# Kernel tuning notes

Hardware: AMD Instinct MI355X
Metric: run time of the kernel (lower is better)

Reference implementation:

```python
import jax, jax.numpy as jnp
import numpy as np

T, H, N = 4096, 2048, 1024  # seq_length, d_model, d_hidden
MAX_PHASE = 6.28


def setup_inputs() -> dict:
    key = jax.random.key(0)
    ks = jax.random.split(key, 9)
    inputs = jax.random.normal(ks[0], (T, H), dtype=jnp.float32)
    # LRU init (exp_param=True, r_min=0, r_max=1): lambda = exp(-exp(nu) + i*exp(theta))
    u1 = jax.random.uniform(ks[1], (N,), dtype=jnp.float32)
    u2 = jax.random.uniform(ks[2], (N,), dtype=jnp.float32)
    nu = jnp.log(-0.5 * jnp.log(u1))            # log-parameterized decay
    theta = jnp.log(MAX_PHASE * u2)             # log-parameterized phase
    # gamma_log = log(sqrt(1 - |lambda|^2)), |lambda| = exp(-exp(nu))
    gamma_log = 0.5 * jnp.log(1.0 - jnp.exp(-2.0 * jnp.exp(nu)) + 1e-8)
    B_re = jax.random.normal(ks[3], (N, H), dtype=jnp.float32) / np.sqrt(2 * H)
    B_im = jax.random.normal(ks[4], (N, H), dtype=jnp.float32) / np.sqrt(2 * H)
    C_re = jax.random.normal(ks[5], (H, N), dtype=jnp.float32) / np.sqrt(N)
    C_im = jax.random.normal(ks[6], (H, N), dtype=jnp.float32) / np.sqrt(N)
    D = jax.random.normal(ks[7], (H,), dtype=jnp.float32)
    return {"inputs": inputs, "nu": nu, "theta": theta, "gamma_log": gamma_log,
            "B_re": B_re, "B_im": B_im, "C_re": C_re, "C_im": C_im, "D": D}


def _binary_operator_diag(q_i, q_j):
    A_i, b_i = q_i
    A_j, b_j = q_j
    return (A_j * A_i, A_j * b_i + b_j)


def reference(inputs, nu, theta, gamma_log, B_re, B_im, C_re, C_im, D):
    # diag_lambda = exp(-exp(nu) + i*exp(theta))   (exp_param=True)
    diag_lambda = jnp.exp(-jnp.exp(nu) + 1j * jnp.exp(theta))      # [N] complex64
    gamma = jnp.exp(gamma_log)                                      # [N]
    B_norm = (B_re + 1j * B_im) * gamma[:, None]                    # [N, H] complex
    # Bu_t = B_norm @ u_t  ->  [T, N]
    Bu = inputs.astype(jnp.complex64) @ B_norm.T
    Lam = jnp.broadcast_to(diag_lambda[None, :], Bu.shape)          # [T, N]
    # parallel scan of diagonal linear recurrence h_t = lambda * h_{t-1} + Bu_t
    _, h = jax.lax.associative_scan(_binary_operator_diag, (Lam, Bu))
    C = C_re + 1j * C_im                                            # [H, N]
    # y_t = Re(C @ h_t) + D * u_t
    y = (h @ C.T).real + D[None, :] * inputs                        # [T, H]
    return y
```

## Files before the change

kernel.cpp:

```cpp
#include <hip/hip_runtime.h>
#include <math.h>

#define T_DIM 4096
#define H_DIM 2048
#define N_DIM 1024
#define N2    2048
#define KK    2048
#define CHUNK 64
#define NCHUNK (T_DIM / CHUNK)
#define NT    (KK / 64)

using u16    = unsigned short;
using u16x4  = __attribute__((ext_vector_type(4))) u16;
using bf16x8 = __attribute__((ext_vector_type(8))) short;
using f32x4  = __attribute__((ext_vector_type(4))) float;

typedef const __attribute__((address_space(1))) u16 glob_u16;
typedef __attribute__((address_space(3))) u16 lds_u16;

__device__ inline void gload16(const u16* g, u16* l) {
    __builtin_amdgcn_global_load_lds((glob_u16*)g, (lds_u16*)l, 16, 0, 0);
}

__device__ inline u16 f2bf(float x) {
    unsigned u = __builtin_bit_cast(unsigned, x);
    u += 0x7fffu + ((u >> 16) & 1u);
    return (u16)(u >> 16);
}
__device__ inline float bf2f(u16 x) {
    return __builtin_bit_cast(float, (unsigned)x << 16);
}

__global__ __launch_bounds__(256) void cvt_u_k(const float* __restrict__ X,
                                               u16* __restrict__ Y) {
    size_t i = ((size_t)blockIdx.x * 256 + threadIdx.x) * 4;
    float4 v = *(const float4*)(X + i);
    u16x4 o = { f2bf(v.x), f2bf(v.y), f2bf(v.z), f2bf(v.w) };
    *(u16x4*)(Y + i) = o;
}

__global__ __launch_bounds__(256) void cvt_b_k(const float* __restrict__ Bre,
                                               const float* __restrict__ Bim,
                                               const float* __restrict__ glog,
                                               u16* __restrict__ Bcat) {
    size_t i = ((size_t)blockIdx.x * 256 + threadIdx.x) * 4;
    int n = (int)(i >> 11);
    size_t h = i & 2047;
    int nn = n & (N_DIM - 1);
    float g = expf(glog[nn]);
    const float* src = (n < N_DIM ? Bre : Bim) + (size_t)nn * H_DIM + h;
    float4 v = *(const float4*)src;
    u16x4 o = { f2bf(v.x * g), f2bf(v.y * g), f2bf(v.z * g), f2bf(v.w * g) };
    *(u16x4*)(Bcat + i) = o;
}

__global__ __launch_bounds__(256) void cvt_c_k(const float* __restrict__ Cre,
                                               const float* __restrict__ Cim,
                                               u16* __restrict__ Ccat) {
    size_t i = ((size_t)blockIdx.x * 256 + threadIdx.x) * 4;
    int hrow = (int)(i >> 11);
    int n = (int)(i & 2047);
    float sgn = 1.f;
    const float* src;
    if (n < N_DIM) src = Cre + (size_t)hrow * N_DIM + n;
    else { src = Cim + (size_t)hrow * N_DIM + (n - N_DIM); sgn = -1.f; }
    float4 v = *(const float4*)src;
    u16x4 o = { f2bf(v.x * sgn), f2bf(v.y * sgn), f2bf(v.z * sgn), f2bf(v.w * sgn) };
    *(u16x4*)(Ccat + i) = o;
}

template <int EPI>
__global__ __launch_bounds__(512, 1) void gemm_pipe(
    const u16* __restrict__ A, const u16* __restrict__ B,
    float* __restrict__ C, const float* __restrict__ D,
    const u16* __restrict__ Ubf)
{
    __shared__ u16 lds[65536];

    const int tid  = threadIdx.x;
    const int wave = tid >> 6, lane = tid & 63;
    const int nbid = (blockIdx.x & 7) * 32 + (blockIdx.x >> 3);
    const int bm = nbid >> 4;
    const int bn = nbid & 15;
    const size_t row0 = (size_t)bm * 256;
    const size_t col0 = (size_t)bn * 128;
    const int wr = wave >> 1, wc = wave & 1;
    const int fr = lane & 15, fq = lane >> 4;

    const int srow = tid >> 3;
    const int skc  = (tid & 7) ^ (srow & 7);
    const u16* aSrc = A + (row0 + srow) * KK + skc * 8;
    const u16* bSrc = B + (col0 + srow) * KK + skc * 8;

    const int aBase = (wr * 64 + fr) * 64;
    const int bBase = (wc * 64 + fr) * 64;
    const int swz0 = ((fq)     ^ (fr & 7)) * 8;
    const int swz1 = ((4 + fq) ^ (fr & 7)) * 8;

    f32x4 acc[4][4] = {};

    auto STAGE_A = [&](int buf, int kt) {
#pragma unroll
        for (int u = 0; u < 4; ++u)
            gload16(aSrc + (size_t)u * 64 * KK + kt * 64,
                    &lds[buf * 16384 + u * 4096 + wave * 512]);
    };
    auto STAGE_B = [&](int buf, int kt) {
#pragma unroll
        for (int u = 0; u < 2; ++u)
            gload16(bSrc + (size_t)u * 64 * KK + kt * 64,
                    &lds[49152 + buf * 8192 + u * 4096 + wave * 512]);
    };

    bf16x8 fa[4], fb[4], ga[4], gb[4];

    auto READ_F = [&](const u16* Ab, const u16* Bb, int swz) {
#pragma unroll
        for (int m = 0; m < 4; ++m) fa[m] = *(const bf16x8*)&Ab[aBase + m * 1024 + swz];
#pragma unroll
        for (int n = 0; n < 4; ++n) fb[n] = *(const bf16x8*)&Bb[bBase + n * 1024 + swz];
    };
    auto READ_G = [&](const u16* Ab, const u16* Bb, int swz) {
#pragma unroll
        for (int m = 0; m < 4; ++m) ga[m] = *(const bf16x8*)&Ab[aBase + m * 1024 + swz];
#pragma unroll
        for (int n = 0; n < 4; ++n) gb[n] = *(const bf16x8*)&Bb[bBase + n * 1024 + swz];
    };
    auto MFMA_F = [&]() {
        __builtin_amdgcn_s_setprio(1);
#pragma unroll
        for (int m = 0; m < 4; ++m)
#pragma unroll
            for (int n = 0; n < 4; ++n)
                acc[m][n] = __builtin_amdgcn_mfma_f32_16x16x32_bf16(
                    fa[m], fb[n], acc[m][n], 0, 0, 0);
        __builtin_amdgcn_s_setprio(0);
    };
    auto MFMA_G = [&]() {
        __builtin_amdgcn_s_setprio(1);
#pragma unroll
        for (int m = 0; m < 4; ++m)
#pragma unroll
            for (int n = 0; n < 4; ++n)
                acc[m][n] = __builtin_amdgcn_mfma_f32_16x16x32_bf16(
                    ga[m], gb[n], acc[m][n], 0, 0, 0);
        __builtin_amdgcn_s_setprio(0);
    };

    STAGE_A(0, 0); STAGE_B(0, 0); STAGE_A(1, 1);
    asm volatile("s_waitcnt vmcnt(4)" ::: "memory");
    __builtin_amdgcn_s_barrier();
    READ_F(&lds[0], &lds[49152], swz0);

    int a_cur = 0;
    for (int t = 0; t < NT; ++t) {
        const u16* Ab = &lds[a_cur * 16384];
        const u16* Bb = &lds[49152 + (t & 1) * 8192];

        if (t + 1 < NT) STAGE_B((t + 1) & 1, t + 1);
        MFMA_F();
        if (t + 2 < NT) {
            int a_nxt = a_cur - 1; if (a_nxt < 0) a_nxt = 2;
            STAGE_A(a_nxt, t + 2);
        }
        READ_G(Ab, Bb, swz1);
        MFMA_G();

        if (t + 1 < NT) {
            if (t + 2 < NT) asm volatile("s_waitcnt vmcnt(4)" ::: "memory");
            else            asm volatile("s_waitcnt vmcnt(0)" ::: "memory");
            __builtin_amdgcn_s_barrier();
            int a_n = a_cur + 1; if (a_n == 3) a_n = 0;
            READ_F(&lds[a_n * 16384], &lds[49152 + ((t + 1) & 1) * 8192], swz0);
        }
        ++a_cur; if (a_cur == 3) a_cur = 0;
    }

    const int crow = (int)row0 + wr * 64 + fq * 4;
    const int ccol = (int)col0 + wc * 64 + fr;
    float dc[4];
    if constexpr (EPI) {
#pragma unroll
        for (int n = 0; n < 4; ++n) dc[n] = D[ccol + n * 16];
    }
#pragma unroll
    for (int m = 0; m < 4; ++m)
#pragma unroll
        for (int n = 0; n < 4; ++n) {
            int cc = ccol + n * 16;
#pragma unroll
            for (int j = 0; j < 4; ++j) {
                int r = crow + m * 16 + j;
                size_t p = (size_t)r * N2 + cc;
                float v = acc[m][n][j];
                if constexpr (EPI) v += dc[n] * bf2f(Ubf[p]);
                C[p] = v;
            }
        }
}

__global__ __launch_bounds__(256) void carry_pass_k(const float* __restrict__ Bu,
                                                    const float* __restrict__ nu,
                                                    const float* __restrict__ theta,
                                                    float* __restrict__ car) {
    int idx = blockIdx.x * 256 + threadIdx.x;
    int chan = idx & (N_DIM - 1);
    int chunk = idx >> 10;
    float a = expf(nu[chan]), b = expf(theta[chan]);
    float m = expf(-a), s, c;
    __sincosf(b, &s, &c);
    float lr = m * c, li = m * s;
    float hr = 0.f, hi = 0.f;
    size_t base = (size_t)chunk * CHUNK * N2 + chan;
    for (int i = 0; i < CHUNK; ++i) {
        size_t p = base + (size_t)i * N2;
        float br = Bu[p], bi = Bu[p + N_DIM];
        float nr = fmaf(lr, hr, fmaf(-li, hi, br));
        float ni = fmaf(lr, hi, fmaf(li, hr, bi));
        hr = nr; hi = ni;
    }
    car[(size_t)chunk * N2 + chan] = hr;
    car[(size_t)chunk * N2 + N_DIM + chan] = hi;
}

__global__ __launch_bounds__(256) void scan_carry_k(float* __restrict__ car,
                                                    const float* __restrict__ nu,
                                                    const float* __restrict__ theta) {
    __shared__ float sR[NCHUNK][65], sI[NCHUNK][65];
    int tid = threadIdx.x;
    int chan0 = blockIdx.x * 64;
    for (int i = tid; i < NCHUNK * 64; i += 256) {
        int ck = i >> 6, c = i & 63;
        sR[ck][c] = car[(size_t)ck * N2 + chan0 + c];
        sI[ck][c] = car[(size_t)ck * N2 + N_DIM + chan0 + c];
    }
    __syncthreads();
    if (tid < 64) {
        int chan = chan0 + tid;
        float a = expf(nu[chan]), b = expf(theta[chan]);
        float m = expf(-(float)CHUNK * a), s, c;
        __sincosf((float)CHUNK * b, &s, &c);
        float lr = m * c, li = m * s;
        float hr = sR[0][tid], hi = sI[0][tid];
        for (int ck = 1; ck < NCHUNK; ++ck) {
            float nr = fmaf(lr, hr, fmaf(-li, hi, sR[ck][tid]));
            float ni = fmaf(lr, hi, fmaf(li, hr, sI[ck][tid]));
            hr = nr; hi = ni;
            sR[ck][tid] = hr; sI[ck][tid] = hi;
        }
    }
    __syncthreads();
    for (int i = tid; i < NCHUNK * 64; i += 256) {
        int ck = i >> 6, c = i & 63;
        car[(size_t)ck * N2 + chan0 + c] = sR[ck][c];
        car[(size_t)ck * N2 + N_DIM + chan0 + c] = sI[ck][c];
    }
}

__global__ __launch_bounds__(256) void scan_out_k(const float* __restrict__ Bu,
                                                  const float* __restrict__ car,
                                                  const float* __restrict__ nu,
                                                  const float* __restrict__ theta,
                                                  u16* __restrict__ Hbf) {
    int idx = blockIdx.x * 256 + threadIdx.x;
    int chan = idx & (N_DIM - 1);
    int chunk = idx >> 10;
    float a = expf(nu[chan]), b = expf(theta[chan]);
    float m = expf(-a), s, c;
    __sincosf(b, &s, &c);
    float lr = m * c, li = m * s;
    float hr = 0.f, hi = 0.f;
    if (chunk > 0) {
        size_t cp = (size_t)(chunk - 1) * N2 + chan;
        hr = car[cp]; hi = car[cp + N_DIM];
    }
    size_t base = (size_t)chunk * CHUNK * N2 + chan;
    for (int i = 0; i < CHUNK; ++i) {
        size_t p = base + (size_t)i * N2;
        float br = Bu[p], bi = Bu[p + N_DIM];
        float nr = fmaf(lr, hr, fmaf(-li, hi, br));
        float ni = fmaf(lr, hi, fmaf(li, hr, bi));
        hr = nr; hi = ni;
        Hbf[p] = f2bf(hr);
        Hbf[p + N_DIM] = f2bf(hi);
    }
}

extern "C" void kernel_launch(void* const* d_in, const int* in_sizes, int n_in,
                              void* d_out, int out_size, void* d_ws, size_t ws_size,
                              hipStream_t stream) {
    const float* U     = (const float*)d_in[0];
    const float* nu    = (const float*)d_in[1];
    const float* theta = (const float*)d_in[2];
    const float* glog  = (const float*)d_in[3];
    const float* Bre   = (const float*)d_in[4];
    const float* Bim   = (const float*)d_in[5];
    const float* Cre   = (const float*)d_in[6];
    const float* Cim   = (const float*)d_in[7];
    const float* Dp    = (const float*)d_in[8];
    float* Y = (float*)d_out;

    u16* Ubf  = (u16*)d_ws;
    u16* Bcat = Ubf + (size_t)T_DIM * H_DIM;
    u16* Ccat = Bcat + (size_t)N2 * H_DIM;
    u16* Hbf  = Ccat + (size_t)H_DIM * N2;
    float* Bu = (float*)(Hbf + (size_t)T_DIM * N2);
    float* car = Bu + (size_t)T_DIM * N2;

    cvt_u_k<<<(T_DIM * H_DIM / 4) / 256, 256, 0, stream>>>(U, Ubf);
    cvt_b_k<<<((size_t)N2 * H_DIM / 4) / 256, 256, 0, stream>>>(Bre, Bim, glog, Bcat);
    cvt_c_k<<<((size_t)H_DIM * N2 / 4) / 256, 256, 0, stream>>>(Cre, Cim, Ccat);

    gemm_pipe<0><<<256, 512, 0, stream>>>(Ubf, Bcat, Bu, nullptr, nullptr);

    carry_pass_k<<<(NCHUNK * N_DIM) / 256, 256, 0, stream>>>(Bu, nu, theta, car);
    scan_carry_k<<<N_DIM / 64, 256, 0, stream>>>(car, nu, theta);
    scan_out_k<<<(NCHUNK * N_DIM) / 256, 256, 0, stream>>>(Bu, car, nu, theta, Hbf);

    gemm_pipe<1><<<256, 512, 0, stream>>>(Hbf, Ccat, Y, Dp, Ubf);
}
```

Baseline: 114.9 us.

## Split K across wave pairs in GEMM with LDS reduction of partial accumulators

The GEMM kernel now assigns the two k-halves of each 64-wide K tile to separate waves. Each wave computes a 128x64 output sub-tile over half the K slice, and the two partial accumulators are reduced through LDS before the epilogue. The F/G double-buffered register prefetch is removed, and launch bounds now request two blocks per SM. The intent is fewer LDS fragment reads per MFMA, since each wave reuses its B fragments across 8 A rows, plus more latency hiding. The costs are higher register pressure (128 accumulator floats per lane), the loss of the register-level prefetch overlap, and an extra LDS reduction with a barrier. The 128KB LDS allocation likely still prevents two blocks from sharing an SM.

```diff
diff --git a/kernel.cpp b/kernel.cpp
--- a/kernel.cpp
+++ b/kernel.cpp
@@ -70,7 +70,7 @@
 }
 
 template <int EPI>
-__global__ __launch_bounds__(512, 1) void gemm_pipe(
+__global__ __launch_bounds__(512, 2) void gemm_pipe(
     const u16* __restrict__ A, const u16* __restrict__ B,
     float* __restrict__ C, const float* __restrict__ D,
     const u16* __restrict__ Ubf)
@@ -84,7 +84,9 @@
     const int bn = nbid & 15;
     const size_t row0 = (size_t)bm * 256;
     const size_t col0 = (size_t)bn * 128;
-    const int wr = wave >> 1, wc = wave & 1;
+    const int kg = wave & 1;
+    const int wc = (wave >> 1) & 1;
+    const int wr = wave >> 2;
     const int fr = lane & 15, fq = lane >> 4;
 
     const int srow = tid >> 3;
@@ -92,12 +94,11 @@
     const u16* aSrc = A + (row0 + srow) * KK + skc * 8;
     const u16* bSrc = B + (col0 + srow) * KK + skc * 8;
 
-    const int aBase = (wr * 64 + fr) * 64;
-    const int bBase = (wc * 64 + fr) * 64;
-    const int swz0 = ((fq)     ^ (fr & 7)) * 8;
-    const int swz1 = ((4 + fq) ^ (fr & 7)) * 8;
-
-    f32x4 acc[4][4] = {};
+    const int slot = ((kg * 4 + fq) ^ (fr & 7)) * 8;
+    const int aOff = (wr * 128 + fr) * 64 + slot;
+    const int bOff = (wc * 64 + fr) * 64 + slot;
+
+    f32x4 acc[8][4] = {};
 
     auto STAGE_A = [&](int buf, int kt) {
 #pragma unroll
@@ -112,91 +113,82 @@
                     &lds[49152 + buf * 8192 + u * 4096 + wave * 512]);
     };
 
-    bf16x8 fa[4], fb[4], ga[4], gb[4];
-
-    auto READ_F = [&](const u16* Ab, const u16* Bb, int swz) {
-#pragma unroll
-        for (int m = 0; m < 4; ++m) fa[m] = *(const bf16x8*)&Ab[aBase + m * 1024 + swz];
-#pragma unroll
-        for (int n = 0; n < 4; ++n) fb[n] = *(const bf16x8*)&Bb[bBase + n * 1024 + swz];
-    };
-    auto READ_G = [&](const u16* Ab, const u16* Bb, int swz) {
-#pragma unroll
-        for (int m = 0; m < 4; ++m) ga[m] = *(const bf16x8*)&Ab[aBase + m * 1024 + swz];
-#pragma unroll
-        for (int n = 0; n < 4; ++n) gb[n] = *(const bf16x8*)&Bb[bBase + n * 1024 + swz];
-    };
-    auto MFMA_F = [&]() {
+    STAGE_A(0, 0); STAGE_B(0, 0); STAGE_A(1, 1);
+    asm volatile("s_waitcnt vmcnt(4)" ::: "memory");
+    __builtin_amdgcn_s_barrier();
+
+    int a_cur = 0;
+    for (int t = 0; t < NT; ++t) {
+        const u16* Ab = &lds[a_cur * 16384];
+        const u16* Bb = &lds[49152 + (t & 1) * 8192];
+
+        bf16x8 fb[4], fa[8];
+#pragma unroll
+        for (int n = 0; n < 4; ++n) fb[n] = *(const bf16x8*)&Bb[bOff + n * 1024];
+#pragma unroll
+        for (int m = 0; m < 8; ++m) fa[m] = *(const bf16x8*)&Ab[aOff + m * 1024];
+
+        if (t + 1 < NT) STAGE_B((t + 1) & 1, t + 1);
+        if (t + 2 < NT) {
+            int a_nxt = a_cur + 2; if (a_nxt >= 3) a_nxt -= 3;
+            STAGE_A(a_nxt, t + 2);
+        }
+
         __builtin_amdgcn_s_setprio(1);
 #pragma unroll
-        for (int m = 0; m < 4; ++m)
+        for (int m = 0; m < 8; ++m)
 #pragma unroll
             for (int n = 0; n < 4; ++n)
                 acc[m][n] = __builtin_amdgcn_mfma_f32_16x16x32_bf16(
                     fa[m], fb[n], acc[m][n], 0, 0, 0);
         __builtin_amdgcn_s_setprio(0);
-    };
-    auto MFMA_G = [&]() {
-        __builtin_amdgcn_s_setprio(1);
-#pragma unroll
-        for (int m = 0; m < 4; ++m)
-#pragma unroll
-            for (int n = 0; n < 4; ++n)
-                acc[m][n] = __builtin_amdgcn_mfma_f32_16x16x32_bf16(
-                    ga[m], gb[n], acc[m][n], 0, 0, 0);
-        __builtin_amdgcn_s_setprio(0);
-    };
-
-    STAGE_A(0, 0); STAGE_B(0, 0); STAGE_A(1, 1);
-    asm volatile("s_waitcnt vmcnt(4)" ::: "memory");
-    __builtin_amdgcn_s_barrier();
-    READ_F(&lds[0], &lds[49152], swz0);
-
-    int a_cur = 0;
-    for (int t = 0; t < NT; ++t) {
-        const u16* Ab = &lds[a_cur * 16384];
-        const u16* Bb = &lds[49152 + (t & 1) * 8192];
-
-        if (t + 1 < NT) STAGE_B((t + 1) & 1, t + 1);
-        MFMA_F();
-        if (t + 2 < NT) {
-            int a_nxt = a_cur - 1; if (a_nxt < 0) a_nxt = 2;
-            STAGE_A(a_nxt, t + 2);
-        }
-        READ_G(Ab, Bb, swz1);
-        MFMA_G();
 
         if (t + 1 < NT) {
             if (t + 2 < NT) asm volatile("s_waitcnt vmcnt(4)" ::: "memory");
             else            asm volatile("s_waitcnt vmcnt(0)" ::: "memory");
             __builtin_amdgcn_s_barrier();
-            int a_n = a_cur + 1; if (a_n == 3) a_n = 0;
-            READ_F(&lds[a_n * 16384], &lds[49152 + ((t + 1) & 1) * 8192], swz0);
         }
         ++a_cur; if (a_cur == 3) a_cur = 0;
     }
 
-    const int crow = (int)row0 + wr * 64 + fq * 4;
-    const int ccol = (int)col0 + wc * 64 + fr;
-    float dc[4];
-    if constexpr (EPI) {
-#pragma unroll
-        for (int n = 0; n < 4; ++n) dc[n] = D[ccol + n * 16];
-    }
-#pragma unroll
-    for (int m = 0; m < 4; ++m)
-#pragma unroll
-        for (int n = 0; n < 4; ++n) {
-            int cc = ccol + n * 16;
-#pragma unroll
-            for (int j = 0; j < 4; ++j) {
-                int r = crow + m * 16 + j;
-                size_t p = (size_t)r * N2 + cc;
-                float v = acc[m][n][j];
-                if constexpr (EPI) v += dc[n] * bf2f(Ubf[p]);
-                C[p] = v;
+    __builtin_amdgcn_s_barrier();
+    const int pair = wr * 2 + wc;
+    float* lf = (float*)lds;
+    if (kg == 1) {
+#pragma unroll
+        for (int i = 0; i < 32; ++i)
+            *(f32x4*)&lf[pair * 8192 + (i * 64 + lane) * 4] = acc[i >> 2][i & 3];
+    }
+    asm volatile("s_waitcnt lgkmcnt(0)" ::: "memory");
+    __builtin_amdgcn_s_barrier();
+    if (kg == 0) {
+#pragma unroll
+        for (int i = 0; i < 32; ++i) {
+            f32x4 o = *(const f32x4*)&lf[pair * 8192 + (i * 64 + lane) * 4];
+            acc[i >> 2][i & 3] += o;
+        }
+        const int crow = (int)row0 + wr * 128 + fq * 4;
+        const int ccol = (int)col0 + wc * 64 + fr;
+        float dc[4];
+        if constexpr (EPI) {
+#pragma unroll
+            for (int n = 0; n < 4; ++n) dc[n] = D[ccol + n * 16];
+        }
+#pragma unroll
+        for (int m = 0; m < 8; ++m)
+#pragma unroll
+            for (int n = 0; n < 4; ++n) {
+                int cc = ccol + n * 16;
+#pragma unroll
+                for (int j = 0; j < 4; ++j) {
+                    int r = crow + m * 16 + j;
+                    size_t p = (size_t)r * N2 + cc;
+                    float v = acc[m][n][j];
+                    if constexpr (EPI) v += dc[n] * bf2f(Ubf[p]);
+                    C[p] = v;
+                }
             }
-        }
+    }
 }
 
 __global__ __launch_bounds__(256) void carry_pass_k(const float* __restrict__ Bu,
```

Result: slower. 122.2 us (+6.3%).

## Shrink GEMM tiles to 128x128 with two blocks per CU and store Bu as bf16

Applied to the files above, without the earlier changes.

The GEMM block tile drops from 256x128 with 512 threads to 128x128 with 256 threads. LDS use falls so two blocks can share a CU, and the grid doubles to 512 blocks with the XCD remap adjusted to match. The first GEMM now writes Bu as bf16 instead of fp32, which halves the traffic for that write and for the two scan kernels that read it. The cost is less reuse per tile and extra rounding error on Bu before the recurrence.

```diff
diff --git a/kernel.cpp b/kernel.cpp
--- a/kernel.cpp
+++ b/kernel.cpp
@@ -70,19 +70,19 @@
 }
 
 template <int EPI>
-__global__ __launch_bounds__(512, 1) void gemm_pipe(
+__global__ __launch_bounds__(256, 2) void gemm_pipe(
     const u16* __restrict__ A, const u16* __restrict__ B,
-    float* __restrict__ C, const float* __restrict__ D,
+    void* __restrict__ Cout, const float* __restrict__ D,
     const u16* __restrict__ Ubf)
 {
-    __shared__ u16 lds[65536];
+    __shared__ u16 lds[40960];
 
     const int tid  = threadIdx.x;
     const int wave = tid >> 6, lane = tid & 63;
-    const int nbid = (blockIdx.x & 7) * 32 + (blockIdx.x >> 3);
+    const int nbid = (blockIdx.x & 7) * 64 + (blockIdx.x >> 3);
     const int bm = nbid >> 4;
     const int bn = nbid & 15;
-    const size_t row0 = (size_t)bm * 256;
+    const size_t row0 = (size_t)bm * 128;
     const size_t col0 = (size_t)bn * 128;
     const int wr = wave >> 1, wc = wave & 1;
     const int fr = lane & 15, fq = lane >> 4;
@@ -92,8 +92,8 @@
     const u16* aSrc = A + (row0 + srow) * KK + skc * 8;
     const u16* bSrc = B + (col0 + srow) * KK + skc * 8;
 
-    const int aBase = (wr * 64 + fr) * 64;
-    const int bBase = (wc * 64 + fr) * 64;
+    const int aOff = (wr * 64 + fr) * 64;
+    const int bOff = (wc * 64 + fr) * 64;
     const int swz0 = ((fq)     ^ (fr & 7)) * 8;
     const int swz1 = ((4 + fq) ^ (fr & 7)) * 8;
 
@@ -102,29 +102,29 @@
     auto STAGE_A = [&](int buf, int kt) {
 #pragma unroll
         for (int u = 0; u < 4; ++u)
-            gload16(aSrc + (size_t)u * 64 * KK + kt * 64,
-                    &lds[buf * 16384 + u * 4096 + wave * 512]);
+            gload16(aSrc + (size_t)u * 32 * KK + kt * 64,
+                    &lds[buf * 8192 + u * 2048 + wave * 512]);
     };
     auto STAGE_B = [&](int buf, int kt) {
 #pragma unroll
-        for (int u = 0; u < 2; ++u)
-            gload16(bSrc + (size_t)u * 64 * KK + kt * 64,
-                    &lds[49152 + buf * 8192 + u * 4096 + wave * 512]);
+        for (int u = 0; u < 4; ++u)
+            gload16(bSrc + (size_t)u * 32 * KK + kt * 64,
+                    &lds[24576 + buf * 8192 + u * 2048 + wave * 512]);
     };
 
     bf16x8 fa[4], fb[4], ga[4], gb[4];
 
     auto READ_F = [&](const u16* Ab, const u16* Bb, int swz) {
 #pragma unroll
-        for (int m = 0; m < 4; ++m) fa[m] = *(const bf16x8*)&Ab[aBase + m * 1024 + swz];
-#pragma unroll
-        for (int n = 0; n < 4; ++n) fb[n] = *(const bf16x8*)&Bb[bBase + n * 1024 + swz];
+        for (int m = 0; m < 4; ++m) fa[m] = *(const bf16x8*)&Ab[aOff + m * 1024 + swz];
+#pragma unroll
+        for (int n = 0; n < 4; ++n) fb[n] = *(const bf16x8*)&Bb[bOff + n * 1024 + swz];
     };
     auto READ_G = [&](const u16* Ab, const u16* Bb, int swz) {
 #pragma unroll
-        for (int m = 0; m < 4; ++m) ga[m] = *(const bf16x8*)&Ab[aBase + m * 1024 + swz];
-#pragma unroll
-        for (int n = 0; n < 4; ++n) gb[n] = *(const bf16x8*)&Bb[bBase + n * 1024 + swz];
+        for (int m = 0; m < 4; ++m) ga[m] = *(const bf16x8*)&Ab[aOff + m * 1024 + swz];
+#pragma unroll
+        for (int n = 0; n < 4; ++n) gb[n] = *(const bf16x8*)&Bb[bOff + n * 1024 + swz];
     };
     auto MFMA_F = [&]() {
         __builtin_amdgcn_s_setprio(1);
@@ -150,17 +150,17 @@
     STAGE_A(0, 0); STAGE_B(0, 0); STAGE_A(1, 1);
     asm volatile("s_waitcnt vmcnt(4)" ::: "memory");
     __builtin_amdgcn_s_barrier();
-    READ_F(&lds[0], &lds[49152], swz0);
+    READ_F(&lds[0], &lds[24576], swz0);
 
     int a_cur = 0;
     for (int t = 0; t < NT; ++t) {
-        const u16* Ab = &lds[a_cur * 16384];
-        const u16* Bb = &lds[49152 + (t & 1) * 8192];
+        const u16* Ab = &lds[a_cur * 8192];
+        const u16* Bb = &lds[24576 + (t & 1) * 8192];
 
         if (t + 1 < NT) STAGE_B((t + 1) & 1, t + 1);
         MFMA_F();
         if (t + 2 < NT) {
-            int a_nxt = a_cur - 1; if (a_nxt < 0) a_nxt = 2;
+            int a_nxt = a_cur + 2; if (a_nxt >= 3) a_nxt -= 3;
             STAGE_A(a_nxt, t + 2);
         }
         READ_G(Ab, Bb, swz1);
@@ -171,7 +171,7 @@
             else            asm volatile("s_waitcnt vmcnt(0)" ::: "memory");
             __builtin_amdgcn_s_barrier();
             int a_n = a_cur + 1; if (a_n == 3) a_n = 0;
-            READ_F(&lds[a_n * 16384], &lds[49152 + ((t + 1) & 1) * 8192], swz0);
+            READ_F(&lds[a_n * 8192], &lds[24576 + ((t + 1) & 1) * 8192], swz0);
         }
         ++a_cur; if (a_cur == 3) a_cur = 0;
     }
@@ -193,13 +193,15 @@
                 int r = crow + m * 16 + j;
                 size_t p = (size_t)r * N2 + cc;
                 float v = acc[m][n][j];
-                if constexpr (EPI) v += dc[n] * bf2f(Ubf[p]);
-                C[p] = v;
+                if constexpr (EPI)
+                    ((float*)Cout)[p] = v + dc[n] * bf2f(Ubf[p]);
+                else
+                    ((u16*)Cout)[p] = f2bf(v);
             }
         }
 }
 
-__global__ __launch_bounds__(256) void carry_pass_k(const float* __restrict__ Bu,
+__global__ __launch_bounds__(256) void carry_pass_k(const u16* __restrict__ Bu,
                                                     const float* __restrict__ nu,
                                                     const float* __restrict__ theta,
                                                     float* __restrict__ car) {
@@ -214,7 +216,7 @@
     size_t base = (size_t)chunk * CHUNK * N2 + chan;
     for (int i = 0; i < CHUNK; ++i) {
         size_t p = base + (size_t)i * N2;
-        float br = Bu[p], bi = Bu[p + N_DIM];
+        float br = bf2f(Bu[p]), bi = bf2f(Bu[p + N_DIM]);
         float nr = fmaf(lr, hr, fmaf(-li, hi, br));
         float ni = fmaf(lr, hi, fmaf(li, hr, bi));
         hr = nr; hi = ni;
@@ -257,7 +259,7 @@
     }
 }
 
-__global__ __launch_bounds__(256) void scan_out_k(const float* __restrict__ Bu,
+__global__ __launch_bounds__(256) void scan_out_k(const u16* __restrict__ Bu,
                                                   const float* __restrict__ car,
                                                   const float* __restrict__ nu,
                                                   const float* __restrict__ theta,
@@ -277,7 +279,7 @@
     size_t base = (size_t)chunk * CHUNK * N2 + chan;
     for (int i = 0; i < CHUNK; ++i) {
         size_t p = base + (size_t)i * N2;
-        float br = Bu[p], bi = Bu[p + N_DIM];
+        float br = bf2f(Bu[p]), bi = bf2f(Bu[p + N_DIM]);
         float nr = fmaf(lr, hr, fmaf(-li, hi, br));
         float ni = fmaf(lr, hi, fmaf(li, hr, bi));
         hr = nr; hi = ni;
@@ -304,18 +306,18 @@
     u16* Bcat = Ubf + (size_t)T_DIM * H_DIM;
     u16* Ccat = Bcat + (size_t)N2 * H_DIM;
     u16* Hbf  = Ccat + (size_t)H_DIM * N2;
-    float* Bu = (float*)(Hbf + (size_t)T_DIM * N2);
-    float* car = Bu + (size_t)T_DIM * N2;
+    u16* Bu   = Hbf + (size_t)T_DIM * N2;
+    float* car = (float*)(Bu + (size_t)T_DIM * N2);
 
     cvt_u_k<<<(T_DIM * H_DIM / 4) / 256, 256, 0, stream>>>(U, Ubf);
     cvt_b_k<<<((size_t)N2 * H_DIM / 4) / 256, 256, 0, stream>>>(Bre, Bim, glog, Bcat);
     cvt_c_k<<<((size_t)H_DIM * N2 / 4) / 256, 256, 0, stream>>>(Cre, Cim, Ccat);
 
-    gemm_pipe<0><<<256, 512, 0, stream>>>(Ubf, Bcat, Bu, nullptr, nullptr);
+    gemm_pipe<0><<<512, 256, 0, stream>>>(Ubf, Bcat, (void*)Bu, nullptr, nullptr);
 
     carry_pass_k<<<(NCHUNK * N_DIM) / 256, 256, 0, stream>>>(Bu, nu, theta, car);
     scan_carry_k<<<N_DIM / 64, 256, 0, stream>>>(car, nu, theta);
     scan_out_k<<<(NCHUNK * N_DIM) / 256, 256, 0, stream>>>(Bu, car, nu, theta, Hbf);
 
-    gemm_pipe<1><<<256, 512, 0, stream>>>(Hbf, Ccat, Y, Dp, Ubf);
-}
+    gemm_pipe<1><<<512, 256, 0, stream>>>(Hbf, Ccat, (void*)Y, Dp, Ubf);
+}
```

New measurement: 114.1 us. About the same (-0.7%).
